# Optimization experiments

Measured on AMD Instinct MI355X. Metric: run time of the kernel, lower is better.

The kernel has to match this reference:

```python
import jax, jax.numpy as jnp
import numpy as np

H, TH, NH, NL, NB = 512, 768, 8, 12, 2
NE, NU, NI, NNZ, K, B = 16000, 2000, 4000, 40000, 10, 64
MD = H // 2
GAMA = 0.1


def _prelu(x, a):
    return jnp.where(x >= 0, x, a * x)


def _spmm(r, c, v, X, n):
    # sparse [n, m] @ X: gather X rows by col index, scale, segment-sum by row.
    return jax.ops.segment_sum(v[:, None] * X[c], r, num_segments=n)


def _forward(systemid, adj_row, adj_col, itemid_set,
             token_embeds, adj_val, node_embeds, user_embedding,
             token_proj_w, token_proj_b, trans_w, trans_b, trans_t_w, trans_t_b,
             meta_w1, meta_b1, meta_w2, meta_b2, sim_w1, sim_w2,
             p1_w1, p1_b1, p1_w2, p1_b2, p2_w, p2_b, prelu_a):
    tok = token_embeds @ token_proj_w + token_proj_b               # [B, H]
    # grouped mean over rows sharing the same system id (vectorized segment-mean)
    same = (systemid[:, None] == systemid[None, :]).astype(tok.dtype)
    group_mean = (same @ tok) / same.sum(1, keepdims=True)         # [B, H]
    filt = _prelu(group_mean @ trans_w + trans_b, prelu_a) * group_mean
    h = jax.nn.relu(filt @ meta_w1 + meta_b1)
    mapping = (h @ meta_w2 + meta_b2).reshape(B, H, H)             # per-sample hypernet weights
    enhanced = jnp.einsum('bh,bhk->bk', user_embedding[systemid], mapping)
    all_tok = user_embedding.at[systemid].set(enhanced)            # [NU, H]
    tok_edge = jnp.zeros_like(user_embedding).at[systemid].set(group_mean)
    # similarity between (enhanced) user/token reps and item reps
    u_rep = all_tok @ sim_w1
    i_rep = node_embeds[itemid_set] @ sim_w2
    u_n = u_rep / jnp.maximum(jnp.linalg.norm(u_rep, axis=1, keepdims=True), 1e-12)
    i_n = i_rep / jnp.maximum(jnp.linalg.norm(i_rep, axis=1, keepdims=True), 1e-12)
    sim = jax.nn.sigmoid(u_n @ i_n.T)                              # [NU, NI]
    tv, ti = jax.lax.top_k(sim, K)
    # combined sparse adjacency = original COO + per-user top-k added edges
    rows = jnp.concatenate([adj_row, jnp.repeat(jnp.arange(NU), K)])
    cols = jnp.concatenate([adj_col, itemid_set[ti].reshape(-1)])
    vals = jnp.concatenate([adj_val, tv.reshape(-1)])
    v_u = vals / jax.ops.segment_sum(vals, rows, num_segments=NU)[rows]   # row-normalized user->item
    v_i = vals / jax.ops.segment_sum(vals, cols, num_segments=NE)[cols]   # row-normalized item->user
    # LightGCN-style 2-layer propagation with multiplicative token gating
    user_tok = _prelu(tok_edge @ trans_t_w + trans_t_b, prelu_a) * tok_edge
    u0, i0 = all_tok, node_embeds
    Ai0 = _spmm(rows, cols, v_u, i0, NU)
    u1 = Ai0 + Ai0 * user_tok
    Att = _spmm(cols, rows, v_i, user_tok, NE)
    i1 = _spmm(cols, rows, v_i, u0, NE) + Att * i0
    Ai1 = _spmm(rows, cols, v_u, i1, NU)
    u2 = Ai1 + Ai1 * user_tok
    i2 = _spmm(cols, rows, v_i, u1, NE) + Att * i1
    user_final = (u0 + u1 + u2) / 3.0
    item_final = (i0 + i1 + i2) / 3.0
    # reconstruction loss vs dense adjacency restricted to item columns
    inv = jnp.full((NE,), -1, jnp.int32).at[itemid_set].set(jnp.arange(NI, dtype=jnp.int32))
    icol = inv[adj_col]
    valid = (icol >= 0).astype(sim.dtype)
    dense = jnp.zeros((NU, NI), sim.dtype).at[adj_row, jnp.maximum(icol, 0)].add(adj_val * valid)
    loss = GAMA * jnp.mean((sim - dense) ** 2)
    # prefix-prompt projection from per-batch system embeddings
    sys_final = user_final[systemid][:, None, :]                   # [B, 1, H]
    p1 = jax.nn.relu(sys_final @ p1_w1 + p1_b1) @ p1_w2 + p1_b2 + sys_final
    p2 = p1 @ p2_w + p2_b
    prompt = p2.reshape(B, 1, NL, NB, NH, H // NH).transpose(2, 3, 0, 4, 1, 5)
    return prompt, item_final, loss


def setup_inputs():
    ks = jax.random.split(jax.random.key(0), 20)
    rng = np.random.default_rng(0)
    s = 0.02
    itemid_set = jnp.asarray(np.sort(rng.choice(NE, NI, replace=False)).astype(np.int32))
    user_embedding = (s * jax.random.normal(ks[4], (NU, H), jnp.float32)).at[0].set(0.0)
    return {
        'systemid': jax.random.randint(ks[0], (B,), 0, NU),
        'adj_row': jax.random.randint(ks[1], (NNZ,), 0, NU),
        'adj_col': jax.random.randint(ks[2], (NNZ,), 0, NE),
        'itemid_set': itemid_set,
        'token_embeds': jax.random.normal(ks[3], (B, TH), jnp.float32),
        'adj_val': jnp.ones((NNZ,), jnp.float32),
        'node_embeds': s * jax.random.normal(ks[5], (NE, H), jnp.float32),
        'user_embedding': user_embedding,
        'token_proj_w': s * jax.random.normal(ks[6], (TH, H), jnp.float32),
        'token_proj_b': jnp.zeros((H,), jnp.float32),
        'trans_w': s * jax.random.normal(ks[7], (H, H), jnp.float32),
        'trans_b': jnp.zeros((H,), jnp.float32),
        'trans_t_w': s * jax.random.normal(ks[8], (H, H), jnp.float32),
        'trans_t_b': jnp.zeros((H,), jnp.float32),
        'meta_w1': s * jax.random.normal(ks[9], (H, MD), jnp.float32),
        'meta_b1': jnp.zeros((MD,), jnp.float32),
        'meta_w2': s * jax.random.normal(ks[10], (MD, H * H), jnp.float32),
        'meta_b2': jnp.zeros((H * H,), jnp.float32),
        'sim_w1': jax.random.normal(ks[11], (H, H), jnp.float32),
        'sim_w2': jax.random.normal(ks[12], (H, H), jnp.float32),
        'p1_w1': s * jax.random.normal(ks[13], (H, MD), jnp.float32),
        'p1_b1': jnp.zeros((MD,), jnp.float32),
        'p1_w2': s * jax.random.normal(ks[14], (MD, H), jnp.float32),
        'p1_b2': jnp.zeros((H,), jnp.float32),
        'p2_w': s * jax.random.normal(ks[15], (H, NL * NB * H), jnp.float32),
        'p2_b': jnp.zeros((NL * NB * H,), jnp.float32),
        'prelu_a': jnp.array(0.25, jnp.float32),
    }


def reference(systemid, adj_row, adj_col, itemid_set, token_embeds, adj_val,
              node_embeds, user_embedding, token_proj_w, token_proj_b,
              trans_w, trans_b, trans_t_w, trans_t_b,
              meta_w1, meta_b1, meta_w2, meta_b2, sim_w1, sim_w2,
              p1_w1, p1_b1, p1_w2, p1_b2, p2_w, p2_b, prelu_a):
    return _forward(systemid, adj_row, adj_col, itemid_set, token_embeds, adj_val,
                    node_embeds, user_embedding, token_proj_w, token_proj_b,
                    trans_w, trans_b, trans_t_w, trans_t_b,
                    meta_w1, meta_b1, meta_w2, meta_b2, sim_w1, sim_w2,
                    p1_w1, p1_b1, p1_w2, p1_b2, p2_w, p2_b, prelu_a)
```

## Files before the change

kernel.cpp:

```cpp
#include <hip/hip_runtime.h>

#define H     512
#define THD   768
#define MDIM  256
#define NE    16000
#define NU    2000
#define NI    4000
#define NNZ   40000
#define KTOP  10
#define NBATCH 64
#define NEDGE 60000
#define GAMA  0.1f
#define P2N   12288
#define PROMPT_N 786432

__device__ __forceinline__ float sigmoidf(float x){ return 1.0f/(1.0f+expf(-x)); }
__device__ __forceinline__ float4 f4z(){ return make_float4(0.f,0.f,0.f,0.f); }

__device__ __forceinline__ void gll16(const float* g, float* l){
  __builtin_amdgcn_global_load_lds(
      (const __attribute__((address_space(1))) void*)g,
      (__attribute__((address_space(3))) void*)l, 16, 0, 0);
}

__global__ void k_tok(const float* __restrict__ A, const float* __restrict__ W,
                      const float* __restrict__ bias, float* __restrict__ C){
  int b=blockIdx.x, c=blockIdx.y*256+threadIdx.x;
  const float* a=A+b*THD; float s=bias[c];
  for(int k=0;k<THD;k++) s+=a[k]*W[k*H+c];
  C[b*H+c]=s;
}

__global__ void k_gm(const int* __restrict__ sysid, const float* __restrict__ tok,
                     float* __restrict__ gm){
  int b=blockIdx.x, c=blockIdx.y*256+threadIdx.x;
  int sid=sysid[b]; float s=0.f, cnt=0.f;
  for(int j=0;j<NBATCH;j++){ if(sysid[j]==sid){ s+=tok[j*H+c]; cnt+=1.f; } }
  gm[b*H+c]=s/cnt;
}

__global__ __launch_bounds__(512) void k_filthh(const float* __restrict__ gm,
        const float* __restrict__ trans_w, const float* __restrict__ trans_b,
        const float* __restrict__ mw1, const float* __restrict__ mb1,
        const float* __restrict__ pa, float* __restrict__ hh){
  __shared__ float fl[512];
  __shared__ float hp[512];
  int b=blockIdx.x, t=threadIdx.x;
  const float* g=gm+b*H;
  float s=trans_b[t];
  for(int k=0;k<H;k++) s+=g[k]*trans_w[k*H+t];
  float al=pa[0]; float pr=(s>=0.f)? s : al*s;
  fl[t]=pr*g[t];
  __syncthreads();
  int m=t&255, half=t>>8;
  float s2=0.f; int k0=half*256;
  for(int k=0;k<256;k++) s2+=fl[k0+k]*mw1[(k0+k)*MDIM+m];
  hp[t]=s2;
  __syncthreads();
  if(t<256) hh[b*MDIM+t]=fmaxf(hp[t]+hp[t+256]+mb1[t],0.f);
}

__global__ void k_uprep(const int* __restrict__ sysid, const float* __restrict__ ue,
                        const float* __restrict__ mb2, float* __restrict__ uesel,
                        float* __restrict__ ueT, float* __restrict__ enh){
  int b=blockIdx.x, c=blockIdx.y*256+threadIdx.x;
  const float* u=ue+(size_t)sysid[b]*H;
  float v=u[c];
  uesel[b*H+c]=v;
  ueT[c*64+b]=v;
  float s=0.f;
  for(int h=0;h<H;h++) s+=u[h]*mb2[(size_t)h*H+c];
  enh[b*H+c]=s;
}

#define HCH 8
__global__ __launch_bounds__(128) void k_big(const float* __restrict__ hh,
        const float* __restrict__ ueT, const float* __restrict__ w2,
        float* __restrict__ partials){
  __shared__ float a_lds[2][HCH][64];
  __shared__ float w_lds[2][HCH][256];
  int m=blockIdx.x;
  int kt=blockIdx.y&1, hs=blockIdx.y>>1;
  int k0=kt*256;
  int hbase=hs*256;
  int t=threadIdx.x;
  int kg=t&15, bg=t>>4;
  const float* w2m = w2 + (size_t)m*(size_t)(H*H);

  float4 acc[8][4];
  #pragma unroll
  for(int r=0;r<8;r++){
    #pragma unroll
    for(int c=0;c<4;c++) acc[r][c]=f4z();
  }

  #define STAGE(buf,hc) do{                                             \
    int h0=hbase+(hc)*HCH;                                              \
    gll16(ueT + (size_t)(h0+(t>>4))*64 + (t&15)*4,                      \
          &a_lds[buf][t>>4][(t&15)*4]);                                 \
    _Pragma("unroll")                                                   \
    for(int j=0;j<4;j++){                                               \
      int i=t+j*128;                                                    \
      gll16(w2m + (size_t)(h0+(i>>6))*H + k0 + (i&63)*4,                \
            &w_lds[buf][i>>6][(i&63)*4]);                               \
    }                                                                   \
  }while(0)

  STAGE(0,0);
  int cur=0;
  for(int hc=0;hc<32;hc++){
    __syncthreads();
    if(hc<31) STAGE(cur^1,hc+1);
    #pragma unroll
    for(int hl=0;hl<HCH;hl++){
      float4 aL=*(const float4*)&a_lds[cur][hl][bg*4];
      float4 aH=*(const float4*)&a_lds[cur][hl][32+bg*4];
      float4 w0=*(const float4*)&w_lds[cur][hl][kg*4];
      float4 w1=*(const float4*)&w_lds[cur][hl][64+kg*4];
      float4 w2v=*(const float4*)&w_lds[cur][hl][128+kg*4];
      float4 w3=*(const float4*)&w_lds[cur][hl][192+kg*4];
      #define FMA4(ac,av,wv) ac.x+=(av)*wv.x; ac.y+=(av)*wv.y; ac.z+=(av)*wv.z; ac.w+=(av)*wv.w;
      #define ROWC(r,av) FMA4(acc[r][0],av,w0) FMA4(acc[r][1],av,w1) FMA4(acc[r][2],av,w2v) FMA4(acc[r][3],av,w3)
      ROWC(0,aL.x) ROWC(1,aL.y) ROWC(2,aL.z) ROWC(3,aL.w)
      ROWC(4,aH.x) ROWC(5,aH.y) ROWC(6,aH.z) ROWC(7,aH.w)
      #undef ROWC
      #undef FMA4
    }
    cur^=1;
  }
  int slice=hs*256+m;
  #pragma unroll
  for(int r=0;r<8;r++){
    int br=(r<4)? (bg*4+r) : (32+bg*4+(r-4));
    float hv=hh[br*MDIM+m];
    float* p=partials+((size_t)slice*NBATCH+br)*H+k0+kg*4;
    *(float4*)(p)    =make_float4(acc[r][0].x*hv,acc[r][0].y*hv,acc[r][0].z*hv,acc[r][0].w*hv);
    *(float4*)(p+64) =make_float4(acc[r][1].x*hv,acc[r][1].y*hv,acc[r][1].z*hv,acc[r][1].w*hv);
    *(float4*)(p+128)=make_float4(acc[r][2].x*hv,acc[r][2].y*hv,acc[r][2].z*hv,acc[r][2].w*hv);
    *(float4*)(p+192)=make_float4(acc[r][3].x*hv,acc[r][3].y*hv,acc[r][3].z*hv,acc[r][3].w*hv);
  }
  #undef STAGE
}

__global__ void k_red1(const float* __restrict__ partials, float* __restrict__ partial2){
  int idx=blockIdx.x*256+threadIdx.x;
  int g=idx>>15, col=idx&32767;
  const float* p=partials+(size_t)g*16*32768+col;
  float s=0.f;
  #pragma unroll
  for(int m=0;m<16;m++) s+=p[(size_t)m*32768];
  partial2[idx]=s;
}
__global__ void k_red2s(const int* __restrict__ sysid, const float* __restrict__ partial2,
                        const float* __restrict__ enh, float* __restrict__ alltok){
  int idx=blockIdx.x*256+threadIdx.x;
  int b=idx>>9, k=idx&511;
  float s=enh[idx];
  #pragma unroll
  for(int g=0;g<32;g++) s+=partial2[(size_t)g*32768+idx];
  alltok[(size_t)sysid[b]*H+k]=s;
}

__global__ void k_user_tok(const int* __restrict__ sysid, const float* __restrict__ gm,
                           const float* __restrict__ W, const float* __restrict__ bias,
                           const float* __restrict__ pa, float* __restrict__ usertok){
  int b=blockIdx.x, c=blockIdx.y*256+threadIdx.x;
  const float* a=gm+b*H; float s=bias[c];
  for(int k=0;k<H;k++) s+=a[k]*W[k*H+c];
  float al=pa[0]; float pr=(s>=0.f)? s : al*s;
  usertok[(size_t)sysid[b]*H+c]=pr*gm[b*H+c];
}

template<int EPI, bool NT, bool AIDX>
__global__ __launch_bounds__(256) void k_gemm(const float* __restrict__ A,
        const float* __restrict__ Bm, const float* __restrict__ bias,
        const int* __restrict__ aidx, float* __restrict__ C, int M, int N, int K){
  __shared__ float As[32][68];
  __shared__ float Bs[32][68];
  int n0=blockIdx.x*64, m0=blockIdx.y*64;
  int t=threadIdx.x;
  int tn=t&15, tm=t>>4;
  float4 pa[2], pb[2];
  #pragma unroll
  for(int i=0;i<2;i++){
    int idx=t+i*256; int r=idx>>3, q=idx&7;
    int grow=m0+r;
    pa[i]=f4z();
    if(grow<M){
      const float* arow=A+(size_t)(AIDX? aidx[grow]:grow)*K;
      pa[i]=*(const float4*)(arow+q*4);
    }
  }
  #pragma unroll
  for(int i=0;i<2;i++){
    if(!NT){
      int idx=t+i*256; int r=idx>>4, q=idx&15;
      pb[i]=*(const float4*)(Bm+(size_t)r*N+n0+q*4);
    } else {
      int idx=t+i*256; int r=idx>>3, q=idx&7;
      int gn=n0+r;
      pb[i]=f4z();
      if(gn<N) pb[i]=*(const float4*)(Bm+(size_t)gn*K+q*4);
    }
  }
  float acc[4][4]={};
  for(int kt=0;kt<K;kt+=32){
    __syncthreads();
    #pragma unroll
    for(int i=0;i<2;i++){
      int idx=t+i*256; int r=idx>>3, q=idx&7;
      As[q*4+0][r]=pa[i].x; As[q*4+1][r]=pa[i].y; As[q*4+2][r]=pa[i].z; As[q*4+3][r]=pa[i].w;
    }
    #pragma unroll
    for(int i=0;i<2;i++){
      if(!NT){
        int idx=t+i*256; int r=idx>>4, q=idx&15;
        *(float4*)&Bs[r][q*4]=pb[i];
      } else {
        int idx=t+i*256; int r=idx>>3, q=idx&7;
        Bs[q*4+0][r]=pb[i].x; Bs[q*4+1][r]=pb[i].y; Bs[q*4+2][r]=pb[i].z; Bs[q*4+3][r]=pb[i].w;
      }
    }
    __syncthreads();
    if(kt+32<K){
      #pragma unroll
      for(int i=0;i<2;i++){
        int idx=t+i*256; int r=idx>>3, q=idx&7;
        int grow=m0+r;
        pa[i]=f4z();
        if(grow<M){
          const float* arow=A+(size_t)(AIDX? aidx[grow]:grow)*K;
          pa[i]=*(const float4*)(arow+kt+32+q*4);
        }
      }
      #pragma unroll
      for(int i=0;i<2;i++){
        if(!NT){
          int idx=t+i*256; int r=idx>>4, q=idx&15;
          pb[i]=*(const float4*)(Bm+(size_t)(kt+32+r)*N+n0+q*4);
        } else {
          int idx=t+i*256; int r=idx>>3, q=idx&7;
          int gn=n0+r;
          pb[i]=f4z();
          if(gn<N) pb[i]=*(const float4*)(Bm+(size_t)gn*K+kt+32+q*4);
        }
      }
    }
    #pragma unroll 8
    for(int k=0;k<32;k++){
      float4 a4=*(const float4*)&As[k][tm*4];
      float4 b4=*(const float4*)&Bs[k][tn*4];
      acc[0][0]+=a4.x*b4.x; acc[0][1]+=a4.x*b4.y; acc[0][2]+=a4.x*b4.z; acc[0][3]+=a4.x*b4.w;
      acc[1][0]+=a4.y*b4.x; acc[1][1]+=a4.y*b4.y; acc[1][2]+=a4.y*b4.z; acc[1][3]+=a4.y*b4.w;
      acc[2][0]+=a4.z*b4.x; acc[2][1]+=a4.z*b4.y; acc[2][2]+=a4.z*b4.z; acc[2][3]+=a4.z*b4.w;
      acc[3][0]+=a4.w*b4.x; acc[3][1]+=a4.w*b4.y; acc[3][2]+=a4.w*b4.z; acc[3][3]+=a4.w*b4.w;
    }
  }
  #pragma unroll
  for(int bi=0;bi<4;bi++){
    int row=m0+tm*4+bi; if(row>=M) continue;
    #pragma unroll
    for(int ki=0;ki<4;ki++){
      int col=n0+tn*4+ki; if(col>=N) continue;
      float v=acc[bi][ki];
      if(EPI==0){ if(bias) v+=bias[col]; }
      else { v=sigmoidf(v); }
      C[(size_t)row*N+col]=v;
    }
  }
}

__global__ __launch_bounds__(512) void k_gemm_sim(const float* __restrict__ A,
        const float* __restrict__ Bm, float* __restrict__ C, int M, int N){
  __shared__ float As[32][132];
  __shared__ float Bs[32][260];
  int n0=blockIdx.x*256, m0=blockIdx.y*128;
  int t=threadIdx.x;
  int tn=t&31, tm=t>>5;
  float4 pa[2], pb[4];
  #pragma unroll
  for(int i=0;i<2;i++){
    int idx=t+i*512; int r=idx>>3, q=idx&7;
    pa[i]=f4z();
    if(m0+r<M) pa[i]=*(const float4*)(A+(size_t)(m0+r)*H+q*4);
  }
  #pragma unroll
  for(int i=0;i<4;i++){
    int idx=t+i*512; int r=idx>>3, q=idx&7;
    pb[i]=f4z();
    if(n0+r<N) pb[i]=*(const float4*)(Bm+(size_t)(n0+r)*H+q*4);
  }
  float4 acc[8][2];
  #pragma unroll
  for(int r=0;r<8;r++){ acc[r][0]=f4z(); acc[r][1]=f4z(); }
  for(int kt=0;kt<H;kt+=32){
    __syncthreads();
    #pragma unroll
    for(int i=0;i<2;i++){
      int idx=t+i*512; int r=idx>>3, q=idx&7;
      As[q*4+0][r]=pa[i].x; As[q*4+1][r]=pa[i].y; As[q*4+2][r]=pa[i].z; As[q*4+3][r]=pa[i].w;
    }
    #pragma unroll
    for(int i=0;i<4;i++){
      int idx=t+i*512; int r=idx>>3, q=idx&7;
      Bs[q*4+0][r]=pb[i].x; Bs[q*4+1][r]=pb[i].y; Bs[q*4+2][r]=pb[i].z; Bs[q*4+3][r]=pb[i].w;
    }
    __syncthreads();
    if(kt+32<H){
      #pragma unroll
      for(int i=0;i<2;i++){
        int idx=t+i*512; int r=idx>>3, q=idx&7;
        pa[i]=f4z();
        if(m0+r<M) pa[i]=*(const float4*)(A+(size_t)(m0+r)*H+kt+32+q*4);
      }
      #pragma unroll
      for(int i=0;i<4;i++){
        int idx=t+i*512; int r=idx>>3, q=idx&7;
        pb[i]=f4z();
        if(n0+r<N) pb[i]=*(const float4*)(Bm+(size_t)(n0+r)*H+kt+32+q*4);
      }
    }
    #pragma unroll 8
    for(int k=0;k<32;k++){
      float4 a0=*(const float4*)&As[k][tm*4];
      float4 a1=*(const float4*)&As[k][64+tm*4];
      float4 b0=*(const float4*)&Bs[k][tn*4];
      float4 b1=*(const float4*)&Bs[k][128+tn*4];
      #define FMA4(ac,av,bv) ac.x+=(av)*bv.x; ac.y+=(av)*bv.y; ac.z+=(av)*bv.z; ac.w+=(av)*bv.w;
      #define ROW(r,av) FMA4(acc[r][0],av,b0) FMA4(acc[r][1],av,b1)
      ROW(0,a0.x) ROW(1,a0.y) ROW(2,a0.z) ROW(3,a0.w)
      ROW(4,a1.x) ROW(5,a1.y) ROW(6,a1.z) ROW(7,a1.w)
      #undef ROW
      #undef FMA4
    }
  }
  #pragma unroll
  for(int r=0;r<8;r++){
    int row=m0+((r<4)? (tm*4+r) : (64+tm*4+(r-4)));
    if(row>=M) continue;
    #pragma unroll
    for(int c=0;c<2;c++){
      int col0=n0+c*128+tn*4;
      float vv[4]={acc[r][c].x,acc[r][c].y,acc[r][c].z,acc[r][c].w};
      #pragma unroll
      for(int j=0;j<4;j++){
        int col=col0+j;
        if(col<N) C[(size_t)row*N+col]=sigmoidf(vv[j]);
      }
    }
  }
}

__global__ __launch_bounds__(256) void k_rownorm(float* __restrict__ X){
  int r=blockIdx.x, t=threadIdx.x;
  float v1=X[(size_t)r*H+t], v2=X[(size_t)r*H+t+256];
  float ss=v1*v1+v2*v2;
  for(int o=32;o;o>>=1) ss+=__shfl_xor(ss,o);
  __shared__ float red[4];
  if((t&63)==0) red[t>>6]=ss;
  __syncthreads();
  float tot=red[0]+red[1]+red[2]+red[3];
  float nrm=fmaxf(sqrtf(tot),1e-12f);
  X[(size_t)r*H+t]=v1/nrm; X[(size_t)r*H+t+256]=v2/nrm;
}

__global__ __launch_bounds__(256) void k_topk(const float* __restrict__ sim,
        float* __restrict__ tv, int* __restrict__ ti){
  __shared__ float rv[4];
  __shared__ int   ri[4];
  int u=blockIdx.x, t=threadIdx.x;
  float v[16];
  #pragma unroll
  for(int j=0;j<16;j++){
    int gi=t+j*256;
    v[j]=(gi<NI)? sim[(size_t)u*NI+gi] : -1e30f;
  }
  for(int k=0;k<KTOP;k++){
    float bv=-1e30f; int bi=1<<30;
    #pragma unroll
    for(int j=0;j<16;j++){
      int gi=t+j*256;
      if(v[j]>bv){ bv=v[j]; bi=gi; }
    }
    #pragma unroll
    for(int o=32;o;o>>=1){
      float ov=__shfl_xor(bv,o); int oi=__shfl_xor(bi,o);
      if(ov>bv || (ov==bv && oi<bi)){ bv=ov; bi=oi; }
    }
    if((t&63)==0){ rv[t>>6]=bv; ri[t>>6]=bi; }
    __syncthreads();
    float fv=rv[0]; int fi=ri[0];
    #pragma unroll
    for(int w=1;w<4;w++){
      float ov=rv[w]; int oi=ri[w];
      if(ov>fv || (ov==fv && oi<fi)){ fv=ov; fi=oi; }
    }
    if(t==0){ tv[u*KTOP+k]=fv; ti[u*KTOP+k]=fi; }
    int jj=fi>>8, tt=fi&255;
    #pragma unroll
    for(int j=0;j<16;j++) if(tt==t && j==jj) v[j]=-1e30f;
    __syncthreads();
  }
}

__global__ void k_edges(const int* __restrict__ adj_row, const int* __restrict__ adj_col,
        const float* __restrict__ adj_val, const int* __restrict__ itemid,
        const float* __restrict__ tv, const int* __restrict__ ti,
        int* __restrict__ rows, int* __restrict__ cols, float* __restrict__ vals,
        float* __restrict__ seg_r, float* __restrict__ seg_c,
        int* __restrict__ row_cnt, int* __restrict__ col_cnt, int* __restrict__ inv){
  int e=blockIdx.x*256+threadIdx.x; if(e>=NEDGE) return;
  if(e<NI) inv[itemid[e]]=e;
  int r,c; float v;
  if(e<NNZ){ r=adj_row[e]; c=adj_col[e]; v=adj_val[e]; }
  else { int x=e-NNZ; int u=x/KTOP; r=u; c=itemid[ti[x]]; v=tv[x]; }
  rows[e]=r; cols[e]=c; vals[e]=v;
  atomicAdd(&seg_r[r],v); atomicAdd(&seg_c[c],v);
  atomicAdd(&row_cnt[r],1); atomicAdd(&col_cnt[c],1);
}

__global__ __launch_bounds__(1024) void k_scan(const int* __restrict__ rc, int* __restrict__ rp,
        const int* __restrict__ cc, int* __restrict__ cp){
  const int* cnt; int* ptr; int n;
  if(blockIdx.x==0){ cnt=rc; ptr=rp; n=NU; } else { cnt=cc; ptr=cp; n=NE; }
  int t=threadIdx.x;
  int chunk=(n+1023)>>10;
  int base=t*chunk;
  int s=0;
  for(int i=0;i<chunk;i++){ int j=base+i; if(j<n) s+=cnt[j]; }
  __shared__ int buf[1024];
  buf[t]=s; __syncthreads();
  for(int off=1;off<1024;off<<=1){
    int y=(t>=off)? buf[t-off]:0;
    __syncthreads();
    buf[t]+=y;
    __syncthreads();
  }
  int run=buf[t]-s;
  for(int i=0;i<chunk;i++){ int j=base+i; if(j<n){ ptr[j]=run; run+=cnt[j]; } }
  if(t==1023) ptr[n]=buf[1023];
}

__global__ void k_fill(const int* __restrict__ rows, const int* __restrict__ cols,
        const float* __restrict__ vals,
        const int* __restrict__ row_ptr, const int* __restrict__ col_ptr,
        const float* __restrict__ seg_r, const float* __restrict__ seg_c,
        int* __restrict__ fr, int* __restrict__ fc,
        int* __restrict__ ebr, int* __restrict__ ebc,
        float* __restrict__ v_u, float* __restrict__ v_i,
        const int* __restrict__ inv, float* __restrict__ dense){
  int e=blockIdx.x*256+threadIdx.x; if(e>=NEDGE) return;
  int r=rows[e], c=cols[e];
  ebr[row_ptr[r]+atomicAdd(&fr[r],1)]=e;
  ebc[col_ptr[c]+atomicAdd(&fc[c],1)]=e;
  v_u[e]=vals[e]/seg_r[r];
  v_i[e]=vals[e]/seg_c[c];
  if(e<NNZ){
    int ic=inv[c];
    if(ic>=0) atomicAdd(&dense[(size_t)r*NI+ic],vals[e]);
  }
}

__global__ __launch_bounds__(256) void k_spmm_u(const int* __restrict__ row_ptr,
        const int* __restrict__ ebr, const int* __restrict__ cols,
        const float* __restrict__ v_u, const float* __restrict__ X,
        const float* __restrict__ usertok, float* __restrict__ out){
  __shared__ int   sc[128];
  __shared__ float sv[128];
  __shared__ float red[3][512];
  int u=blockIdx.x;
  int t=threadIdx.x, w=t>>6, l=t&63;
  int s=row_ptr[u], n=row_ptr[u+1]-s;
  float4 a0=f4z(), a1=f4z();
  for(int base=0;base<n;base+=128){
    int cnt=min(n-base,128);
    if(t<cnt){ int e=ebr[s+base+t]; sc[t]=cols[e]; sv[t]=v_u[e]; }
    __syncthreads();
    for(int j=w;j<cnt;j+=4){
      float v=sv[j];
      const float4* xr=(const float4*)(X+(size_t)sc[j]*H);
      float4 x0=xr[l], x1=xr[l+64];
      a0.x+=v*x0.x; a0.y+=v*x0.y; a0.z+=v*x0.z; a0.w+=v*x0.w;
      a1.x+=v*x1.x; a1.y+=v*x1.y; a1.z+=v*x1.z; a1.w+=v*x1.w;
    }
    __syncthreads();
  }
  if(w>0){ *(float4*)&red[w-1][l*4]=a0; *(float4*)&red[w-1][l*4+256]=a1; }
  __syncthreads();
  if(w==0){
    #pragma unroll
    for(int ww=0;ww<3;ww++){
      float4 r0=*(const float4*)&red[ww][l*4], r1=*(const float4*)&red[ww][l*4+256];
      a0.x+=r0.x; a0.y+=r0.y; a0.z+=r0.z; a0.w+=r0.w;
      a1.x+=r1.x; a1.y+=r1.y; a1.z+=r1.z; a1.w+=r1.w;
    }
    const float4* ut=(const float4*)(usertok+(size_t)u*H);
    float4 u0=ut[l], u1=ut[l+64];
    float4* o=(float4*)(out+(size_t)u*H);
    o[l]   =make_float4(a0.x+a0.x*u0.x, a0.y+a0.y*u0.y, a0.z+a0.z*u0.z, a0.w+a0.w*u0.w);
    o[l+64]=make_float4(a1.x+a1.x*u1.x, a1.y+a1.y*u1.y, a1.z+a1.z*u1.z, a1.w+a1.w*u1.w);
  }
}

__global__ __launch_bounds__(256) void k_spmm_i1(const int* __restrict__ col_ptr,
        const int* __restrict__ ebc, const int* __restrict__ rows,
        const float* __restrict__ v_i, const float* __restrict__ alltok,
        const float* __restrict__ usertok, const float* __restrict__ i0,
        float* __restrict__ Att, float* __restrict__ i1){
  int i=blockIdx.x*4+(threadIdx.x>>6);
  int l=threadIdx.x&63;
  int s=col_ptr[i], e1=col_ptr[i+1];
  float4 aA0=f4z(),aA1=f4z(),aU0=f4z(),aU1=f4z();
  for(int j=s;j<e1;j++){
    int e=ebc[j]; float v=v_i[e]; int r=rows[e];
    const float4* ur=(const float4*)(usertok+(size_t)r*H);
    const float4* ar=(const float4*)(alltok+(size_t)r*H);
    float4 u0=ur[l],u1v=ur[l+64],A0=ar[l],A1=ar[l+64];
    aA0.x+=v*u0.x; aA0.y+=v*u0.y; aA0.z+=v*u0.z; aA0.w+=v*u0.w;
    aA1.x+=v*u1v.x; aA1.y+=v*u1v.y; aA1.z+=v*u1v.z; aA1.w+=v*u1v.w;
    aU0.x+=v*A0.x; aU0.y+=v*A0.y; aU0.z+=v*A0.z; aU0.w+=v*A0.w;
    aU1.x+=v*A1.x; aU1.y+=v*A1.y; aU1.z+=v*A1.z; aU1.w+=v*A1.w;
  }
  size_t o=(size_t)i*128;
  const float4* z=(const float4*)i0;
  float4 z0=z[o+l], z1=z[o+l+64];
  ((float4*)Att)[o+l]   =aA0;
  ((float4*)Att)[o+l+64]=aA1;
  ((float4*)i1)[o+l]   =make_float4(aU0.x+aA0.x*z0.x, aU0.y+aA0.y*z0.y, aU0.z+aA0.z*z0.z, aU0.w+aA0.w*z0.w);
  ((float4*)i1)[o+l+64]=make_float4(aU1.x+aA1.x*z1.x, aU1.y+aA1.y*z1.y, aU1.z+aA1.z*z1.z, aU1.w+aA1.w*z1.w);
}

__global__ __launch_bounds__(256) void k_spmm_i2(const int* __restrict__ col_ptr,
        const int* __restrict__ ebc, const int* __restrict__ rows,
        const float* __restrict__ v_i, const float* __restrict__ u1,
        const float* __restrict__ Att, const float* __restrict__ i1,
        const float* __restrict__ i0, float* __restrict__ item_out){
  int i=blockIdx.x*4+(threadIdx.x>>6);
  int l=threadIdx.x&63;
  int s=col_ptr[i], e1=col_ptr[i+1];
  float4 a0=f4z(), a1=f4z();
  for(int j=s;j<e1;j++){
    int e=ebc[j]; float v=v_i[e];
    const float4* ur=(const float4*)(u1+(size_t)rows[e]*H);
    float4 x0=ur[l], x1=ur[l+64];
    a0.x+=v*x0.x; a0.y+=v*x0.y; a0.z+=v*x0.z; a0.w+=v*x0.w;
    a1.x+=v*x1.x; a1.y+=v*x1.y; a1.z+=v*x1.z; a1.w+=v*x1.w;
  }
  size_t o=(size_t)i*128;
  float4 A0=((const float4*)Att)[o+l], A1=((const float4*)Att)[o+l+64];
  float4 I0=((const float4*)i1)[o+l],  I1=((const float4*)i1)[o+l+64];
  float4 Z0=((const float4*)i0)[o+l],  Z1=((const float4*)i0)[o+l+64];
  float4 r0=make_float4((Z0.x+I0.x+a0.x+A0.x*I0.x)/3.f,(Z0.y+I0.y+a0.y+A0.y*I0.y)/3.f,
                        (Z0.z+I0.z+a0.z+A0.z*I0.z)/3.f,(Z0.w+I0.w+a0.w+A0.w*I0.w)/3.f);
  float4 r1=make_float4((Z1.x+I1.x+a1.x+A1.x*I1.x)/3.f,(Z1.y+I1.y+a1.y+A1.y*I1.y)/3.f,
                        (Z1.z+I1.z+a1.z+A1.z*I1.z)/3.f,(Z1.w+I1.w+a1.w+A1.w*I1.w)/3.f);
  ((float4*)item_out)[o+l]=r0;
  ((float4*)item_out)[o+l+64]=r1;
}

__global__ __launch_bounds__(256) void k_loss(const float* __restrict__ sim,
        const float* __restrict__ dense, float* __restrict__ acc){
  size_t n4=(size_t)NU*NI/4;
  float s=0.f;
  for(size_t i=(size_t)blockIdx.x*256+threadIdx.x; i<n4; i+=(size_t)gridDim.x*256){
    float4 a=((const float4*)sim)[i], d=((const float4*)dense)[i];
    float dx=a.x-d.x, dy=a.y-d.y, dz=a.z-d.z, dw=a.w-d.w;
    s+=dx*dx+dy*dy+dz*dz+dw*dw;
  }
  __shared__ float red[256];
  red[threadIdx.x]=s; __syncthreads();
  for(int o=128;o;o>>=1){ if(threadIdx.x<o) red[threadIdx.x]+=red[threadIdx.x+o]; __syncthreads(); }
  if(threadIdx.x==0) atomicAdd(acc,red[0]);
}
__global__ void k_loss_write(const float* __restrict__ acc, float* __restrict__ out){
  out[0]=GAMA*(acc[0]/(float)((size_t)NU*NI));
}

__global__ __launch_bounds__(512) void k_sysq_p1(const int* __restrict__ sysid,
        const float* __restrict__ u0, const float* __restrict__ u1, const float* __restrict__ u2,
        const float* __restrict__ p1w1, const float* __restrict__ p1b1,
        const float* __restrict__ p1w2, const float* __restrict__ p1b2,
        float* __restrict__ p1buf){
  __shared__ float sf[512];
  __shared__ float hp[512];
  __shared__ float qv[256];
  int b=blockIdx.x, t=threadIdx.x;
  size_t o=(size_t)sysid[b]*H+t;
  float sfv=(u0[o]+u1[o]+u2[o])/3.0f;
  sf[t]=sfv;
  __syncthreads();
  int m=t&255, half=t>>8;
  float s=0.f; int k0=half*256;
  for(int k=0;k<256;k++) s+=sf[k0+k]*p1w1[(k0+k)*MDIM+m];
  hp[t]=s;
  __syncthreads();
  if(t<256) qv[t]=fmaxf(hp[t]+hp[t+256]+p1b1[t],0.f);
  __syncthreads();
  float s2=p1b2[t];
  for(int k=0;k<256;k++) s2+=qv[k]*p1w2[k*H+t];
  p1buf[b*H+t]=s2+sf[t];
}

__global__ void k_perm(const float* __restrict__ p2, float* __restrict__ out){
  int idx=blockIdx.x*256+threadIdx.x;
  int x=idx&511;
  int b=(idx>>9)&63;
  int c=idx>>15;
  out[idx]=p2[(size_t)b*P2N+c*512+x];
}

extern "C" void kernel_launch(void* const* d_in, const int* in_sizes, int n_in,
                              void* d_out, int out_size, void* d_ws, size_t ws_size,
                              hipStream_t stream){
  const int*   sysid   =(const int*)  d_in[0];
  const int*   adj_row =(const int*)  d_in[1];
  const int*   adj_col =(const int*)  d_in[2];
  const int*   itemid  =(const int*)  d_in[3];
  const float* tok_emb =(const float*)d_in[4];
  const float* adj_val =(const float*)d_in[5];
  const float* node_emb=(const float*)d_in[6];
  const float* user_emb=(const float*)d_in[7];
  const float* tp_w    =(const float*)d_in[8];
  const float* tp_b    =(const float*)d_in[9];
  const float* trans_w =(const float*)d_in[10];
  const float* trans_b =(const float*)d_in[11];
  const float* trt_w   =(const float*)d_in[12];
  const float* trt_b   =(const float*)d_in[13];
  const float* mw1     =(const float*)d_in[14];
  const float* mb1     =(const float*)d_in[15];
  const float* mw2     =(const float*)d_in[16];
  const float* mb2     =(const float*)d_in[17];
  const float* sw1     =(const float*)d_in[18];
  const float* sw2     =(const float*)d_in[19];
  const float* p1w1    =(const float*)d_in[20];
  const float* p1b1    =(const float*)d_in[21];
  const float* p1w2    =(const float*)d_in[22];
  const float* p1b2    =(const float*)d_in[23];
  const float* p2w     =(const float*)d_in[24];
  const float* p2b     =(const float*)d_in[25];
  const float* pa      =(const float*)d_in[26];

  float* out_prompt=(float*)d_out;
  float* out_item  =out_prompt+PROMPT_N;
  float* out_loss  =out_item+(size_t)NE*H;

  char* ws=(char*)d_ws; size_t off=0;
  auto A=[&](size_t bytes)->char*{ char* p=ws+off; off+=(bytes+255)&~(size_t)255; return p; };
  float* tok     =(float*)A((size_t)NBATCH*H*4);
  float* gm      =(float*)A((size_t)NBATCH*H*4);
  float* hh      =(float*)A((size_t)NBATCH*MDIM*4);
  float* uesel   =(float*)A((size_t)NBATCH*H*4);
  float* ueT     =(float*)A((size_t)H*NBATCH*4);
  float* enh     =(float*)A((size_t)NBATCH*H*4);
  float* irep    =(float*)A((size_t)NI*H*4);
  float* alltok  =(float*)A((size_t)NU*H*4);
  float* urep    =(float*)A((size_t)NU*H*4);
  float* u1      =(float*)A((size_t)NU*H*4);
  float* u2      =(float*)A((size_t)NU*H*4);
  float* big     =(float*)A((size_t)17825792*4);
  float* partials=big;
  float* partial2=big+16777216;
  float* sim     =big;
  float* dense   =big+8000000;
  float* Att     =big;
  float* i1      =big+8192000;
  float* tv      =(float*)A((size_t)NU*KTOP*4);
  int*   ti      =(int*)  A((size_t)NU*KTOP*4);
  int*   rowsA   =(int*)  A((size_t)NEDGE*4);
  int*   colsA   =(int*)  A((size_t)NEDGE*4);
  float* valsA   =(float*)A((size_t)NEDGE*4);
  float* v_u     =(float*)A((size_t)NEDGE*4);
  float* v_i     =(float*)A((size_t)NEDGE*4);
  int*   ebr     =(int*)  A((size_t)NEDGE*4);
  int*   ebc     =(int*)  A((size_t)NEDGE*4);
  int*   row_ptr =(int*)  A((size_t)(NU+1)*4);
  int*   col_ptr =(int*)  A((size_t)(NE+1)*4);
  size_t zb_bytes=(size_t)NU*H*4 + (size_t)(NU+NE)*4*3 + 256;
  char*  zb      =A(zb_bytes);
  float* usertok =(float*)zb;
  float* seg_r   =usertok+(size_t)NU*H;
  float* seg_c   =seg_r+NU;
  int*   row_cnt =(int*)(seg_c+NE);
  int*   col_cnt =row_cnt+NU;
  int*   fr      =col_cnt+NE;
  int*   fc      =fr+NU;
  float* loss_acc=(float*)(fc+NE);
  int*   inv     =(int*)  A((size_t)NE*4);
  float* p1buf   =(float*)A((size_t)NBATCH*H*4);
  float* p2buf   =(float*)A((size_t)NBATCH*P2N*4);
  (void)ws_size; (void)n_in; (void)in_sizes; (void)out_size;

  dim3 g642(NBATCH,2);

  hipMemcpyAsync(alltok,user_emb,(size_t)NU*H*4,hipMemcpyDeviceToDevice,stream);
  hipMemsetAsync(zb,0,zb_bytes,stream);
  hipMemsetAsync(inv,0xFF,(size_t)NE*4,stream);
  hipMemsetAsync(dense,0,(size_t)8000000*4,stream);

  k_tok   <<<g642,256,0,stream>>>(tok_emb,tp_w,tp_b,tok);
  k_gm    <<<g642,256,0,stream>>>(sysid,tok,gm);
  k_filthh<<<NBATCH,512,0,stream>>>(gm,trans_w,trans_b,mw1,mb1,pa,hh);
  k_uprep <<<g642,256,0,stream>>>(sysid,user_emb,mb2,uesel,ueT,enh);
  k_big   <<<dim3(256,4),128,0,stream>>>(hh,ueT,mw2,partials);
  k_red1  <<<4096,256,0,stream>>>(partials,partial2);
  k_red2s <<<128,256,0,stream>>>(sysid,partial2,enh,alltok);
  k_user_tok<<<g642,256,0,stream>>>(sysid,gm,trt_w,trt_b,pa,usertok);

  k_gemm<0,false,false><<<dim3(8,32),256,0,stream>>>(alltok,sw1,nullptr,nullptr,urep,NU,H,H);
  k_gemm<0,false,true> <<<dim3(8,63),256,0,stream>>>(node_emb,sw2,nullptr,itemid,irep,NI,H,H);
  k_rownorm<<<NU,256,0,stream>>>(urep);
  k_rownorm<<<NI,256,0,stream>>>(irep);
  k_gemm_sim<<<dim3(16,16),512,0,stream>>>(urep,irep,sim,NU,NI);
  k_topk<<<NU,256,0,stream>>>(sim,tv,ti);

  k_edges<<<(NEDGE+255)/256,256,0,stream>>>(adj_row,adj_col,adj_val,itemid,tv,ti,
                                            rowsA,colsA,valsA,seg_r,seg_c,row_cnt,col_cnt,inv);
  k_scan<<<2,1024,0,stream>>>(row_cnt,row_ptr,col_cnt,col_ptr);
  k_fill<<<(NEDGE+255)/256,256,0,stream>>>(rowsA,colsA,valsA,row_ptr,col_ptr,seg_r,seg_c,
                                           fr,fc,ebr,ebc,v_u,v_i,inv,dense);

  k_loss<<<2048,256,0,stream>>>(sim,dense,loss_acc);
  k_loss_write<<<1,1,0,stream>>>(loss_acc,out_loss);

  k_spmm_u <<<NU,256,0,stream>>>(row_ptr,ebr,colsA,v_u,node_emb,usertok,u1);
  k_spmm_i1<<<NE/4,256,0,stream>>>(col_ptr,ebc,rowsA,v_i,alltok,usertok,node_emb,Att,i1);
  k_spmm_u <<<NU,256,0,stream>>>(row_ptr,ebr,colsA,v_u,i1,usertok,u2);
  k_spmm_i2<<<NE/4,256,0,stream>>>(col_ptr,ebc,rowsA,v_i,u1,Att,i1,node_emb,out_item);

  k_sysq_p1<<<NBATCH,512,0,stream>>>(sysid,alltok,u1,u2,p1w1,p1b1,p1w2,p1b2,p1buf);
  k_gemm<0,false,false><<<dim3(192,1),256,0,stream>>>(p1buf,p2w,p2b,nullptr,p2buf,NBATCH,P2N,H);
  k_perm<<<PROMPT_N/256,256,0,stream>>>(p2buf,out_prompt);
}
```

Baseline: 812.8 us.

## Horizontally fuse independent kernels into combined launches and de-alias scratch buffers

Independent kernels now share launches, with the block index choosing the work: filter/hypernet, user prep and user-token go into k_front; the two rep GEMMs into k_gemm_ui; the two rownorms into one kernel; loss with the first SpMM pair; and the second SpMM pair together. This cuts launch count and lets small, underfilled kernels run concurrently on the GPU. Because loss now runs alongside writes to Att, scratch buffers that used to alias the big region get their own allocations, which raises workspace memory use. The unused uesel write is also dropped.

```diff
diff --git a/kernel.cpp b/kernel.cpp
--- a/kernel.cpp
+++ b/kernel.cpp
@@ -13,6 +13,7 @@
 #define GAMA  0.1f
 #define P2N   12288
 #define PROMPT_N 786432
+#define NLOSSB 2048
 
 __device__ __forceinline__ float sigmoidf(float x){ return 1.0f/(1.0f+expf(-x)); }
 __device__ __forceinline__ float4 f4z(){ return make_float4(0.f,0.f,0.f,0.f); }
@@ -39,38 +40,44 @@
   gm[b*H+c]=s/cnt;
 }
 
-__global__ __launch_bounds__(512) void k_filthh(const float* __restrict__ gm,
+__global__ __launch_bounds__(512) void k_front(const int* __restrict__ sysid,
+        const float* __restrict__ gm,
         const float* __restrict__ trans_w, const float* __restrict__ trans_b,
         const float* __restrict__ mw1, const float* __restrict__ mb1,
-        const float* __restrict__ pa, float* __restrict__ hh){
+        const float* __restrict__ ue, const float* __restrict__ mb2,
+        const float* __restrict__ trt_w, const float* __restrict__ trt_b,
+        const float* __restrict__ pa,
+        float* __restrict__ hh, float* __restrict__ ueT, float* __restrict__ enh,
+        float* __restrict__ usertok){
   __shared__ float fl[512];
   __shared__ float hp[512];
-  int b=blockIdx.x, t=threadIdx.x;
-  const float* g=gm+b*H;
-  float s=trans_b[t];
-  for(int k=0;k<H;k++) s+=g[k]*trans_w[k*H+t];
-  float al=pa[0]; float pr=(s>=0.f)? s : al*s;
-  fl[t]=pr*g[t];
-  __syncthreads();
-  int m=t&255, half=t>>8;
-  float s2=0.f; int k0=half*256;
-  for(int k=0;k<256;k++) s2+=fl[k0+k]*mw1[(k0+k)*MDIM+m];
-  hp[t]=s2;
-  __syncthreads();
-  if(t<256) hh[b*MDIM+t]=fmaxf(hp[t]+hp[t+256]+mb1[t],0.f);
-}
-
-__global__ void k_uprep(const int* __restrict__ sysid, const float* __restrict__ ue,
-                        const float* __restrict__ mb2, float* __restrict__ uesel,
-                        float* __restrict__ ueT, float* __restrict__ enh){
-  int b=blockIdx.x, c=blockIdx.y*256+threadIdx.x;
-  const float* u=ue+(size_t)sysid[b]*H;
-  float v=u[c];
-  uesel[b*H+c]=v;
-  ueT[c*64+b]=v;
-  float s=0.f;
-  for(int h=0;h<H;h++) s+=u[h]*mb2[(size_t)h*H+c];
-  enh[b*H+c]=s;
+  int b=blockIdx.x, t=threadIdx.x, which=blockIdx.y;
+  if(which==0){
+    const float* g=gm+b*H;
+    float s=trans_b[t];
+    for(int k=0;k<H;k++) s+=g[k]*trans_w[k*H+t];
+    float al=pa[0]; float pr=(s>=0.f)? s : al*s;
+    fl[t]=pr*g[t];
+    __syncthreads();
+    int m=t&255, half=t>>8;
+    float s2=0.f; int k0=half*256;
+    for(int k=0;k<256;k++) s2+=fl[k0+k]*mw1[(k0+k)*MDIM+m];
+    hp[t]=s2;
+    __syncthreads();
+    if(t<256) hh[b*MDIM+t]=fmaxf(hp[t]+hp[t+256]+mb1[t],0.f);
+  } else if(which==1){
+    const float* u=ue+(size_t)sysid[b]*H;
+    float v=u[t];
+    ueT[t*64+b]=v;
+    float s=0.f;
+    for(int h=0;h<H;h++) s+=u[h]*mb2[(size_t)h*H+t];
+    enh[b*H+t]=s;
+  } else {
+    const float* a=gm+b*H; float s=trt_b[t];
+    for(int k=0;k<H;k++) s+=a[k]*trt_w[k*H+t];
+    float al=pa[0]; float pr=(s>=0.f)? s : al*s;
+    usertok[(size_t)sysid[b]*H+t]=pr*gm[b*H+t];
+  }
 }
 
 #define HCH 8
@@ -161,23 +168,12 @@
   alltok[(size_t)sysid[b]*H+k]=s;
 }
 
-__global__ void k_user_tok(const int* __restrict__ sysid, const float* __restrict__ gm,
-                           const float* __restrict__ W, const float* __restrict__ bias,
-                           const float* __restrict__ pa, float* __restrict__ usertok){
-  int b=blockIdx.x, c=blockIdx.y*256+threadIdx.x;
-  const float* a=gm+b*H; float s=bias[c];
-  for(int k=0;k<H;k++) s+=a[k]*W[k*H+c];
-  float al=pa[0]; float pr=(s>=0.f)? s : al*s;
-  usertok[(size_t)sysid[b]*H+c]=pr*gm[b*H+c];
-}
-
 template<int EPI, bool NT, bool AIDX>
-__global__ __launch_bounds__(256) void k_gemm(const float* __restrict__ A,
-        const float* __restrict__ Bm, const float* __restrict__ bias,
-        const int* __restrict__ aidx, float* __restrict__ C, int M, int N, int K){
-  __shared__ float As[32][68];
-  __shared__ float Bs[32][68];
-  int n0=blockIdx.x*64, m0=blockIdx.y*64;
+__device__ __forceinline__ void gemm_body(float (*As)[68], float (*Bs)[68],
+        const float* __restrict__ A, const float* __restrict__ Bm,
+        const float* __restrict__ bias, const int* __restrict__ aidx,
+        float* __restrict__ C, int M, int N, int K, int bx, int by){
+  int n0=bx*64, m0=by*64;
   int t=threadIdx.x;
   int tn=t&15, tm=t>>4;
   float4 pa[2], pb[2];
@@ -270,6 +266,27 @@
   }
 }
 
+template<int EPI, bool NT, bool AIDX>
+__global__ __launch_bounds__(256) void k_gemm(const float* __restrict__ A,
+        const float* __restrict__ Bm, const float* __restrict__ bias,
+        const int* __restrict__ aidx, float* __restrict__ C, int M, int N, int K){
+  __shared__ float As[32][68];
+  __shared__ float Bs[32][68];
+  gemm_body<EPI,NT,AIDX>(As,Bs,A,Bm,bias,aidx,C,M,N,K,blockIdx.x,blockIdx.y);
+}
+
+__global__ __launch_bounds__(256) void k_gemm_ui(const float* __restrict__ alltok,
+        const float* __restrict__ node_emb, const float* __restrict__ sw1,
+        const float* __restrict__ sw2, const int* __restrict__ itemid,
+        float* __restrict__ urep, float* __restrict__ irep){
+  __shared__ float As[32][68];
+  __shared__ float Bs[32][68];
+  if(blockIdx.y<32)
+    gemm_body<0,false,false>(As,Bs,alltok,sw1,nullptr,nullptr,urep,NU,H,H,blockIdx.x,blockIdx.y);
+  else
+    gemm_body<0,false,true >(As,Bs,node_emb,sw2,nullptr,itemid,irep,NI,H,H,blockIdx.x,blockIdx.y-32);
+}
+
 __global__ __launch_bounds__(512) void k_gemm_sim(const float* __restrict__ A,
         const float* __restrict__ Bm, float* __restrict__ C, int M, int N){
   __shared__ float As[32][132];
@@ -351,9 +368,10 @@
   }
 }
 
-__global__ __launch_bounds__(256) void k_rownorm(float* __restrict__ X){
+__global__ __launch_bounds__(256) void k_rownorm2(float* __restrict__ U, float* __restrict__ I){
   int r=blockIdx.x, t=threadIdx.x;
-  float v1=X[(size_t)r*H+t], v2=X[(size_t)r*H+t+256];
+  float* X=(r<NU)? U+(size_t)r*H : I+(size_t)(r-NU)*H;
+  float v1=X[t], v2=X[t+256];
   float ss=v1*v1+v2*v2;
   for(int o=32;o;o>>=1) ss+=__shfl_xor(ss,o);
   __shared__ float red[4];
@@ -361,7 +379,7 @@
   __syncthreads();
   float tot=red[0]+red[1]+red[2]+red[3];
   float nrm=fmaxf(sqrtf(tot),1e-12f);
-  X[(size_t)r*H+t]=v1/nrm; X[(size_t)r*H+t+256]=v2/nrm;
+  X[t]=v1/nrm; X[t+256]=v2/nrm;
 }
 
 __global__ __launch_bounds__(256) void k_topk(const float* __restrict__ sim,
@@ -461,14 +479,11 @@
   }
 }
 
-__global__ __launch_bounds__(256) void k_spmm_u(const int* __restrict__ row_ptr,
+__device__ __forceinline__ void spmm_u_body(int u, const int* __restrict__ row_ptr,
         const int* __restrict__ ebr, const int* __restrict__ cols,
         const float* __restrict__ v_u, const float* __restrict__ X,
-        const float* __restrict__ usertok, float* __restrict__ out){
-  __shared__ int   sc[128];
-  __shared__ float sv[128];
-  __shared__ float red[3][512];
-  int u=blockIdx.x;
+        const float* __restrict__ usertok, float* __restrict__ out,
+        int* sc, float* sv, float (*red)[512]){
   int t=threadIdx.x, w=t>>6, l=t&63;
   int s=row_ptr[u], n=row_ptr[u+1]-s;
   float4 a0=f4z(), a1=f4z();
@@ -502,12 +517,12 @@
   }
 }
 
-__global__ __launch_bounds__(256) void k_spmm_i1(const int* __restrict__ col_ptr,
+__device__ __forceinline__ void spmm_i1_body(int ib, const int* __restrict__ col_ptr,
         const int* __restrict__ ebc, const int* __restrict__ rows,
         const float* __restrict__ v_i, const float* __restrict__ alltok,
         const float* __restrict__ usertok, const float* __restrict__ i0,
         float* __restrict__ Att, float* __restrict__ i1){
-  int i=blockIdx.x*4+(threadIdx.x>>6);
+  int i=ib*4+(threadIdx.x>>6);
   int l=threadIdx.x&63;
   int s=col_ptr[i], e1=col_ptr[i+1];
   float4 aA0=f4z(),aA1=f4z(),aU0=f4z(),aU1=f4z();
@@ -530,12 +545,12 @@
   ((float4*)i1)[o+l+64]=make_float4(aU1.x+aA1.x*z1.x, aU1.y+aA1.y*z1.y, aU1.z+aA1.z*z1.z, aU1.w+aA1.w*z1.w);
 }
 
-__global__ __launch_bounds__(256) void k_spmm_i2(const int* __restrict__ col_ptr,
+__device__ __forceinline__ void spmm_i2_body(int ib, const int* __restrict__ col_ptr,
         const int* __restrict__ ebc, const int* __restrict__ rows,
         const float* __restrict__ v_i, const float* __restrict__ u1,
         const float* __restrict__ Att, const float* __restrict__ i1,
         const float* __restrict__ i0, float* __restrict__ item_out){
-  int i=blockIdx.x*4+(threadIdx.x>>6);
+  int i=ib*4+(threadIdx.x>>6);
   int l=threadIdx.x&63;
   int s=col_ptr[i], e1=col_ptr[i+1];
   float4 a0=f4z(), a1=f4z();
@@ -558,20 +573,55 @@
   ((float4*)item_out)[o+l+64]=r1;
 }
 
-__global__ __launch_bounds__(256) void k_loss(const float* __restrict__ sim,
-        const float* __restrict__ dense, float* __restrict__ acc){
+__device__ __forceinline__ void loss_body(int lb, const float* __restrict__ sim,
+        const float* __restrict__ dense, float* __restrict__ acc, float* red){
+  int t=threadIdx.x;
   size_t n4=(size_t)NU*NI/4;
   float s=0.f;
-  for(size_t i=(size_t)blockIdx.x*256+threadIdx.x; i<n4; i+=(size_t)gridDim.x*256){
+  for(size_t i=(size_t)lb*256+t; i<n4; i+=(size_t)NLOSSB*256){
     float4 a=((const float4*)sim)[i], d=((const float4*)dense)[i];
     float dx=a.x-d.x, dy=a.y-d.y, dz=a.z-d.z, dw=a.w-d.w;
     s+=dx*dx+dy*dy+dz*dz+dw*dw;
   }
-  __shared__ float red[256];
-  red[threadIdx.x]=s; __syncthreads();
-  for(int o=128;o;o>>=1){ if(threadIdx.x<o) red[threadIdx.x]+=red[threadIdx.x+o]; __syncthreads(); }
-  if(threadIdx.x==0) atomicAdd(acc,red[0]);
-}
+  red[t]=s; __syncthreads();
+  for(int o=128;o;o>>=1){ if(t<o) red[t]+=red[t+o]; __syncthreads(); }
+  if(t==0) atomicAdd(acc,red[0]);
+}
+
+__global__ __launch_bounds__(256) void k_stage1(const int* __restrict__ row_ptr,
+        const int* __restrict__ ebr, const int* __restrict__ colsA,
+        const float* __restrict__ v_u, const float* __restrict__ node_emb,
+        const float* __restrict__ usertok, float* __restrict__ u1,
+        const int* __restrict__ col_ptr, const int* __restrict__ ebc,
+        const int* __restrict__ rowsA, const float* __restrict__ v_i,
+        const float* __restrict__ alltok, float* __restrict__ Att, float* __restrict__ i1,
+        const float* __restrict__ sim, const float* __restrict__ dense,
+        float* __restrict__ loss_acc){
+  __shared__ int   sc[128];
+  __shared__ float sv[128];
+  __shared__ float red[3][512];
+  int bid=blockIdx.x;
+  if(bid<NU)              spmm_u_body(bid,row_ptr,ebr,colsA,v_u,node_emb,usertok,u1,sc,sv,red);
+  else if(bid<NU+NE/4)    spmm_i1_body(bid-NU,col_ptr,ebc,rowsA,v_i,alltok,usertok,node_emb,Att,i1);
+  else                    loss_body(bid-(NU+NE/4),sim,dense,loss_acc,(float*)red);
+}
+
+__global__ __launch_bounds__(256) void k_stage2(const int* __restrict__ row_ptr,
+        const int* __restrict__ ebr, const int* __restrict__ colsA,
+        const float* __restrict__ v_u, const float* __restrict__ i1,
+        const float* __restrict__ usertok, float* __restrict__ u2,
+        const int* __restrict__ col_ptr, const int* __restrict__ ebc,
+        const int* __restrict__ rowsA, const float* __restrict__ v_i,
+        const float* __restrict__ u1, const float* __restrict__ Att,
+        const float* __restrict__ node_emb, float* __restrict__ item_out){
+  __shared__ int   sc[128];
+  __shared__ float sv[128];
+  __shared__ float red[3][512];
+  int bid=blockIdx.x;
+  if(bid<NU) spmm_u_body(bid,row_ptr,ebr,colsA,v_u,i1,usertok,u2,sc,sv,red);
+  else       spmm_i2_body(bid-NU,col_ptr,ebc,rowsA,v_i,u1,Att,i1,node_emb,item_out);
+}
+
 __global__ void k_loss_write(const float* __restrict__ acc, float* __restrict__ out){
   out[0]=GAMA*(acc[0]/(float)((size_t)NU*NI));
 }
@@ -649,7 +699,6 @@
   float* tok     =(float*)A((size_t)NBATCH*H*4);
   float* gm      =(float*)A((size_t)NBATCH*H*4);
   float* hh      =(float*)A((size_t)NBATCH*MDIM*4);
-  float* uesel   =(float*)A((size_t)NBATCH*H*4);
   float* ueT     =(float*)A((size_t)H*NBATCH*4);
   float* enh     =(float*)A((size_t)NBATCH*H*4);
   float* irep    =(float*)A((size_t)NI*H*4);
@@ -657,13 +706,12 @@
   float* urep    =(float*)A((size_t)NU*H*4);
   float* u1      =(float*)A((size_t)NU*H*4);
   float* u2      =(float*)A((size_t)NU*H*4);
-  float* big     =(float*)A((size_t)17825792*4);
-  float* partials=big;
-  float* partial2=big+16777216;
-  float* sim     =big;
-  float* dense   =big+8000000;
-  float* Att     =big;
-  float* i1      =big+8192000;
+  float* partials=(float*)A((size_t)512*NBATCH*H*4);
+  float* partial2=(float*)A((size_t)32*32768*4);
+  float* sim     =(float*)A((size_t)NU*NI*4);
+  float* dense   =(float*)A((size_t)NU*NI*4);
+  float* Att     =(float*)A((size_t)NE*H*4);
+  float* i1      =(float*)A((size_t)NE*H*4);
   float* tv      =(float*)A((size_t)NU*KTOP*4);
   int*   ti      =(int*)  A((size_t)NU*KTOP*4);
   int*   rowsA   =(int*)  A((size_t)NEDGE*4);
@@ -690,26 +738,22 @@
   float* p2buf   =(float*)A((size_t)NBATCH*P2N*4);
   (void)ws_size; (void)n_in; (void)in_sizes; (void)out_size;
 
-  dim3 g642(NBATCH,2);
-
   hipMemcpyAsync(alltok,user_emb,(size_t)NU*H*4,hipMemcpyDeviceToDevice,stream);
   hipMemsetAsync(zb,0,zb_bytes,stream);
   hipMemsetAsync(inv,0xFF,(size_t)NE*4,stream);
-  hipMemsetAsync(dense,0,(size_t)8000000*4,stream);
-
-  k_tok   <<<g642,256,0,stream>>>(tok_emb,tp_w,tp_b,tok);
-  k_gm    <<<g642,256,0,stream>>>(sysid,tok,gm);
-  k_filthh<<<NBATCH,512,0,stream>>>(gm,trans_w,trans_b,mw1,mb1,pa,hh);
-  k_uprep <<<g642,256,0,stream>>>(sysid,user_emb,mb2,uesel,ueT,enh);
-  k_big   <<<dim3(256,4),128,0,stream>>>(hh,ueT,mw2,partials);
-  k_red1  <<<4096,256,0,stream>>>(partials,partial2);
-  k_red2s <<<128,256,0,stream>>>(sysid,partial2,enh,alltok);
-  k_user_tok<<<g642,256,0,stream>>>(sysid,gm,trt_w,trt_b,pa,usertok);
-
-  k_gemm<0,false,false><<<dim3(8,32),256,0,stream>>>(alltok,sw1,nullptr,nullptr,urep,NU,H,H);
-  k_gemm<0,false,true> <<<dim3(8,63),256,0,stream>>>(node_emb,sw2,nullptr,itemid,irep,NI,H,H);
-  k_rownorm<<<NU,256,0,stream>>>(urep);
-  k_rownorm<<<NI,256,0,stream>>>(irep);
+  hipMemsetAsync(dense,0,(size_t)NU*NI*4,stream);
+
+  k_tok  <<<dim3(NBATCH,2),256,0,stream>>>(tok_emb,tp_w,tp_b,tok);
+  k_gm   <<<dim3(NBATCH,2),256,0,stream>>>(sysid,tok,gm);
+  k_front<<<dim3(NBATCH,3),512,0,stream>>>(sysid,gm,trans_w,trans_b,mw1,mb1,
+                                           user_emb,mb2,trt_w,trt_b,pa,
+                                           hh,ueT,enh,usertok);
+  k_big  <<<dim3(256,4),128,0,stream>>>(hh,ueT,mw2,partials);
+  k_red1 <<<4096,256,0,stream>>>(partials,partial2);
+  k_red2s<<<128,256,0,stream>>>(sysid,partial2,enh,alltok);
+
+  k_gemm_ui<<<dim3(8,95),256,0,stream>>>(alltok,node_emb,sw1,sw2,itemid,urep,irep);
+  k_rownorm2<<<NU+NI,256,0,stream>>>(urep,irep);
   k_gemm_sim<<<dim3(16,16),512,0,stream>>>(urep,irep,sim,NU,NI);
   k_topk<<<NU,256,0,stream>>>(sim,tv,ti);
 
@@ -719,13 +763,13 @@
   k_fill<<<(NEDGE+255)/256,256,0,stream>>>(rowsA,colsA,valsA,row_ptr,col_ptr,seg_r,seg_c,
                                            fr,fc,ebr,ebc,v_u,v_i,inv,dense);
 
-  k_loss<<<2048,256,0,stream>>>(sim,dense,loss_acc);
+  k_stage1<<<NU+NE/4+NLOSSB,256,0,stream>>>(row_ptr,ebr,colsA,v_u,node_emb,usertok,u1,
+                                            col_ptr,ebc,rowsA,v_i,alltok,Att,i1,
+                                            sim,dense,loss_acc);
   k_loss_write<<<1,1,0,stream>>>(loss_acc,out_loss);
 
-  k_spmm_u <<<NU,256,0,stream>>>(row_ptr,ebr,colsA,v_u,node_emb,usertok,u1);
-  k_spmm_i1<<<NE/4,256,0,stream>>>(col_ptr,ebc,rowsA,v_i,alltok,usertok,node_emb,Att,i1);
-  k_spmm_u <<<NU,256,0,stream>>>(row_ptr,ebr,colsA,v_u,i1,usertok,u2);
-  k_spmm_i2<<<NE/4,256,0,stream>>>(col_ptr,ebc,rowsA,v_i,u1,Att,i1,node_emb,out_item);
+  k_stage2<<<NU+NE/4,256,0,stream>>>(row_ptr,ebr,colsA,v_u,i1,usertok,u2,
+                                     col_ptr,ebc,rowsA,v_i,u1,Att,node_emb,out_item);
 
   k_sysq_p1<<<NBATCH,512,0,stream>>>(sysid,alltok,u1,u2,p1w1,p1b1,p1w2,p1b2,p1buf);
   k_gemm<0,false,false><<<dim3(192,1),256,0,stream>>>(p1buf,p2w,p2b,nullptr,p2buf,NBATCH,P2N,H);
```

Result: faster. 700.8 us (-13.8%).
